# Performance work log

Measured on AMD Instinct MI355X. Metric: run time of the kernel, lower is better.

Reference implementation:

```python
import jax, jax.numpy as jnp
import numpy as np

B, N, DIM = 4, 2048, 256
H, HD, M = 8, 32, 4
SPARSE_TOPK = 32


def setup_inputs() -> dict:
    key = jax.random.key(0)
    ks = jax.random.split(key, 6)
    x = jax.random.normal(ks[0], (B, N, DIM), dtype=jnp.float32)
    w_qkv = jax.random.normal(ks[1], (DIM, 3 * H * HD), dtype=jnp.float32) * 0.02
    b_qkv = jnp.zeros((3 * H * HD,), dtype=jnp.float32)
    w_proj = jax.random.normal(ks[2], (H * HD, DIM), dtype=jnp.float32) * 0.02
    b_proj = jnp.zeros((DIM,), dtype=jnp.float32)
    scale = jnp.ones((1, H, 1, 1), dtype=jnp.float32)  # trainable scale, init scale_value=1.0
    mem_k = jax.random.normal(ks[3], (H, M, HD), dtype=jnp.float32)
    mem_v = jax.random.normal(ks[4], (H, M, HD), dtype=jnp.float32)
    return {"x": x, "w_qkv": w_qkv, "b_qkv": b_qkv, "w_proj": w_proj,
            "b_proj": b_proj, "scale": scale, "mem_k": mem_k, "mem_v": mem_v}


def reference(x, w_qkv, b_qkv, w_proj, b_proj, scale, mem_k, mem_v):
    b, n, dim = x.shape
    h, m, hd = mem_k.shape
    qkv = (x @ w_qkv + b_qkv).reshape(b, n, 3, h, hd).transpose(2, 0, 3, 1, 4)
    q, k, v = qkv[0], qkv[1], qkv[2]
    # concat memory vectors along key-length axis -> [B,H,N+M,hd]
    k = jnp.concatenate([k, jnp.broadcast_to(mem_k, (b, h, m, hd))], axis=2)
    v = jnp.concatenate([v, jnp.broadcast_to(mem_v, (b, h, m, hd))], axis=2)
    s = n + m
    # scores with trainable per-head scale: [B,H,N,S]
    scores = jnp.einsum('bhnd,bhsd->bhns', q, k) * (hd ** -0.5) * scale
    neg = -jnp.finfo(scores.dtype).max
    # improve_locality: mask rectangular diagonal (eye(N, S))
    diag = jnp.arange(n)[:, None] == jnp.arange(s)[None, :]
    scores = jnp.where(diag, neg, scores)
    # sparse topk: keep only values >= k-th largest per row
    top = jax.lax.top_k(scores, SPARSE_TOPK)[0]
    vk = top[..., -1:]
    scores = jnp.where(scores < vk, neg, scores)
    attn = jax.nn.softmax(scores, axis=-1)
    out = jnp.einsum('bhns,bhsd->bhnd', attn, v)
    out = out.transpose(0, 2, 1, 3).reshape(b, n, h * hd)
    return out @ w_proj + b_proj
```

## Files before the change

kernel.cpp:

```cpp
#include <hip/hip_runtime.h>
#include <float.h>
#include <stdint.h>

#define Bb   4
#define Nn   2048
#define DIMc 256
#define Hh   8
#define HDd  32
#define Mm   4
#define STOT 2052
#define ROWS 8
#define SROW 2112
#define NVROW 2052

typedef float f32x2 __attribute__((ext_vector_type(2)));

__device__ __forceinline__ unsigned int f2key(float s) {
    unsigned int b = __float_as_uint(s);
    return (b & 0x80000000u) ? ~b : (b | 0x80000000u);
}
__device__ __forceinline__ float key2f(unsigned int u) {
    unsigned int b = (u & 0x80000000u) ? (u ^ 0x80000000u) : ~u;
    return __uint_as_float(b);
}

__global__ __launch_bounds__(256) void sgemm_qkv(
    const float* __restrict__ A, const float* __restrict__ Bm,
    const float* __restrict__ bias, float* __restrict__ Qb,
    float* __restrict__ kTb, float* __restrict__ Vx,
    const float* __restrict__ memv)
{
    __shared__ __align__(16) float As[16][68];
    __shared__ __align__(16) float Bs[16][64];
    __shared__ __align__(16) float Ts[64][65];
    const int tid = threadIdx.x;
    const int tx = tid & 15, ty = tid >> 4;
    const int m0 = blockIdx.y * 64, n0 = blockIdx.x * 64;
    const int arow = tid >> 2, acol = (tid & 3) * 4;
    const int brow = tid >> 4, bcol = (tid & 15) * 4;
    float acc[4][4] = {};
    for (int kb = 0; kb < DIMc; kb += 16) {
        const float4 av = *(const float4*)&A[(size_t)(m0 + arow) * DIMc + kb + acol];
        const float4 bv = *(const float4*)&Bm[(size_t)(kb + brow) * 768 + n0 + bcol];
        __syncthreads();
        As[acol + 0][arow] = av.x;
        As[acol + 1][arow] = av.y;
        As[acol + 2][arow] = av.z;
        As[acol + 3][arow] = av.w;
        *(float4*)&Bs[brow][bcol] = bv;
        __syncthreads();
#pragma unroll
        for (int k = 0; k < 16; ++k) {
            const float4 a  = *(const float4*)&As[k][ty * 4];
            const float4 bq = *(const float4*)&Bs[k][tx * 4];
            const float aa[4] = {a.x, a.y, a.z, a.w};
            const float bb[4] = {bq.x, bq.y, bq.z, bq.w};
#pragma unroll
            for (int i = 0; i < 4; ++i)
#pragma unroll
                for (int j = 0; j < 4; ++j)
                    acc[i][j] = fmaf(aa[i], bb[j], acc[i][j]);
        }
    }
    const float4 bv = *(const float4*)&bias[n0 + tx * 4];
    const float bb[4] = {bv.x, bv.y, bv.z, bv.w};
    const int path = n0 >> 8;
    if (path == 1) {
#pragma unroll
        for (int i = 0; i < 4; ++i)
#pragma unroll
            for (int j = 0; j < 4; ++j)
                Ts[tx * 4 + j][ty * 4 + i] = acc[i][j] + bb[j];
        __syncthreads();
        const int c_local = tid >> 2;
        const int seg     = tid & 3;
        const int cg = (n0 - 256) + c_local;
        const int hh = cg >> 5, dd = cg & 31;
        const int bi = m0 >> 11, j0 = (m0 & 2047) + seg * 16;
        float* dst = kTb + (((size_t)(bi * Hh + hh) * HDd + dd) * Nn) + j0;
#pragma unroll
        for (int q = 0; q < 4; ++q)
            *(float4*)(dst + q * 4) = *(const float4*)&Ts[c_local][seg * 16 + q * 4];
    } else if (path == 0) {
        const int c0 = n0 + tx * 4;
#pragma unroll
        for (int i = 0; i < 4; ++i) {
            float4 o;
            o.x = acc[i][0] + bb[0];
            o.y = acc[i][1] + bb[1];
            o.z = acc[i][2] + bb[2];
            o.w = acc[i][3] + bb[3];
            *(float4*)&Qb[(size_t)(m0 + ty * 4 + i) * 256 + c0] = o;
        }
    } else {
        const int c0 = (n0 & 255) + tx * 4;
        const size_t row_base = (size_t)(m0 >> 11) * NVROW + (m0 & 2047);
#pragma unroll
        for (int i = 0; i < 4; ++i) {
            float4 o;
            o.x = acc[i][0] + bb[0];
            o.y = acc[i][1] + bb[1];
            o.z = acc[i][2] + bb[2];
            o.w = acc[i][3] + bb[3];
            *(float4*)&Vx[(row_base + ty * 4 + i) * 256 + c0] = o;
        }
        if (n0 == 512 && (m0 & 2047) == 0) {
            const int bb2 = m0 >> 11;
#pragma unroll
            for (int mm = 0; mm < Mm; ++mm)
                Vx[((size_t)bb2 * NVROW + Nn + mm) * 256 + tid] =
                    memv[((tid >> 5) * Mm + mm) * HDd + (tid & 31)];
        }
    }
}

__global__ __launch_bounds__(256) void sgemm_bias(
    const float* __restrict__ A, const float* __restrict__ Bm,
    const float* __restrict__ bias, float* __restrict__ C,
    int Md, int Nd, int Kd)
{
    __shared__ __align__(16) float As[16][68];
    __shared__ __align__(16) float Bs[16][64];
    const int tid = threadIdx.x;
    const int tx = tid & 15, ty = tid >> 4;
    const int m0 = blockIdx.y * 64, n0 = blockIdx.x * 64;
    const int arow = tid >> 2, acol = (tid & 3) * 4;
    const int brow = tid >> 4, bcol = (tid & 15) * 4;
    float acc[4][4] = {};
    for (int kb = 0; kb < Kd; kb += 16) {
        const float4 av = *(const float4*)&A[(size_t)(m0 + arow) * Kd + kb + acol];
        const float4 bv = *(const float4*)&Bm[(size_t)(kb + brow) * Nd + n0 + bcol];
        __syncthreads();
        As[acol + 0][arow] = av.x;
        As[acol + 1][arow] = av.y;
        As[acol + 2][arow] = av.z;
        As[acol + 3][arow] = av.w;
        *(float4*)&Bs[brow][bcol] = bv;
        __syncthreads();
#pragma unroll
        for (int k = 0; k < 16; ++k) {
            const float4 a  = *(const float4*)&As[k][ty * 4];
            const float4 bq = *(const float4*)&Bs[k][tx * 4];
            const float aa[4] = {a.x, a.y, a.z, a.w};
            const float bb[4] = {bq.x, bq.y, bq.z, bq.w};
#pragma unroll
            for (int i = 0; i < 4; ++i)
#pragma unroll
                for (int j = 0; j < 4; ++j)
                    acc[i][j] = fmaf(aa[i], bb[j], acc[i][j]);
        }
    }
    const float4 bv = *(const float4*)&bias[n0 + tx * 4];
    const float bb[4] = {bv.x, bv.y, bv.z, bv.w};
#pragma unroll
    for (int i = 0; i < 4; ++i) {
        float4 o;
        o.x = acc[i][0] + bb[0];
        o.y = acc[i][1] + bb[1];
        o.z = acc[i][2] + bb[2];
        o.w = acc[i][3] + bb[3];
        *(float4*)&C[(size_t)(m0 + ty * 4 + i) * Nd + n0 + tx * 4] = o;
    }
}

#if __has_builtin(__builtin_elementwise_fma)
#define PKSTEP(Q, P)                                                        \
    { const f32x2 qq = {(Q), (Q)};                                          \
      a01 = __builtin_elementwise_fma(qq, ((const f32x2*)&kd[P])[0], a01);  \
      a23 = __builtin_elementwise_fma(qq, ((const f32x2*)&kd[P])[1], a23); }
#else
#define PKSTEP(Q, P)                                                        \
    { a01.x = fmaf((Q), kd[P].x, a01.x); a01.y = fmaf((Q), kd[P].y, a01.y); \
      a23.x = fmaf((Q), kd[P].z, a23.x); a23.y = fmaf((Q), kd[P].w, a23.y); }
#endif

__global__ __launch_bounds__(512, 4) void attn_sparse(
    const float* __restrict__ Qb, const float* __restrict__ kTb,
    const float* __restrict__ Vx, const float* __restrict__ memk,
    const float* __restrict__ scale, float* __restrict__ attn_out)
{
    __shared__ __align__(16) unsigned int S[ROWS][SROW];
    __shared__ __align__(16) float qs[ROWS][HDd];
    __shared__ unsigned int       u_list[ROWS][64];
    __shared__ unsigned short     j_list[ROWS][64];
    __shared__ unsigned long long wj_list[ROWS][64];

    const int tid    = threadIdx.x;
    const int ntiles = Nn / ROWS;
    const int tile   = blockIdx.x % ntiles;
    const int h      = (blockIdx.x / ntiles) % Hh;
    const int b      = blockIdx.x / (ntiles * Hh);
    const int n0     = tile * ROWS;
    const float sc   = scale[h] * 0.17677669529663688f;

    if (tid < ROWS * HDd) {
        const int r = tid >> 5, d2 = tid & 31;
        qs[r][d2] = Qb[(size_t)(b * Nn + n0 + r) * 256 + h * HDd + d2];
    }
    __syncthreads();

    const float* kT = kTb + (size_t)(b * Hh + h) * (HDd * Nn);

    {
        const int j0 = tid * 4;
        f32x2 acc01[ROWS], acc23[ROWS];
#pragma unroll
        for (int r = 0; r < ROWS; ++r) { acc01[r] = (f32x2){0.f, 0.f}; acc23[r] = (f32x2){0.f, 0.f}; }
#pragma unroll 1
        for (int dc = 0; dc < 4; ++dc) {
            float4 kd[8];
#pragma unroll
            for (int dd = 0; dd < 8; ++dd)
                kd[dd] = *(const float4*)&kT[(dc * 8 + dd) * Nn + j0];
#pragma unroll
            for (int r = 0; r < ROWS; ++r) {
                const float4 qa = *(const float4*)&qs[r][dc * 8];
                const float4 qb2 = *(const float4*)&qs[r][dc * 8 + 4];
                f32x2 a01 = acc01[r], a23 = acc23[r];
                PKSTEP(qa.x, 0) PKSTEP(qa.y, 1) PKSTEP(qa.z, 2) PKSTEP(qa.w, 3)
                PKSTEP(qb2.x, 4) PKSTEP(qb2.y, 5) PKSTEP(qb2.z, 6) PKSTEP(qb2.w, 7)
                acc01[r] = a01; acc23[r] = a23;
            }
        }
#pragma unroll
        for (int r = 0; r < ROWS; ++r) {
            const float af[4] = {acc01[r].x, acc01[r].y, acc23[r].x, acc23[r].y};
            uint4 o;
            unsigned int* op = (unsigned int*)&o;
#pragma unroll
            for (int kk = 0; kk < 4; ++kk) {
                float s = af[kk] * sc;
                if (j0 + kk == n0 + r) s = -FLT_MAX;
                op[kk] = f2key(s);
            }
            *(uint4*)&S[r][j0] = o;
        }
    }
    if (tid < 16) {
        const int j0 = 2048 + tid * 4;
        float acc[ROWS][4];
#pragma unroll
        for (int r = 0; r < ROWS; ++r)
#pragma unroll
            for (int kk = 0; kk < 4; ++kk) acc[r][kk] = 0.f;
        const float* kp[4];
#pragma unroll
        for (int kk = 0; kk < 4; ++kk) {
            const int j = j0 + kk;
            kp[kk] = (j < STOT) ? (memk + (size_t)(h * Mm + (j - Nn)) * HDd)
                                : memk;
        }
#pragma unroll 1
        for (int dc = 0; dc < 4; ++dc) {
            float4 k0[4], k1[4];
#pragma unroll
            for (int kk = 0; kk < 4; ++kk) {
                k0[kk] = *(const float4*)(kp[kk] + dc * 8);
                k1[kk] = *(const float4*)(kp[kk] + dc * 8 + 4);
            }
#pragma unroll
            for (int r = 0; r < ROWS; ++r) {
                const float4 qa = *(const float4*)&qs[r][dc * 8];
                const float4 qb2 = *(const float4*)&qs[r][dc * 8 + 4];
#pragma unroll
                for (int kk = 0; kk < 4; ++kk) {
                    float t = fmaf(qa.x, k0[kk].x, acc[r][kk]);
                    t = fmaf(qa.y, k0[kk].y, t);
                    t = fmaf(qa.z, k0[kk].z, t);
                    t = fmaf(qa.w, k0[kk].w, t);
                    t = fmaf(qb2.x, k1[kk].x, t);
                    t = fmaf(qb2.y, k1[kk].y, t);
                    t = fmaf(qb2.z, k1[kk].z, t);
                    t = fmaf(qb2.w, k1[kk].w, t);
                    acc[r][kk] = t;
                }
            }
        }
#pragma unroll
        for (int r = 0; r < ROWS; ++r) {
            uint4 o;
            unsigned int* op = (unsigned int*)&o;
#pragma unroll
            for (int kk = 0; kk < 4; ++kk) {
                const int j = j0 + kk;
                float s = acc[r][kk] * sc;
                if (j >= STOT || j == n0 + r) s = -FLT_MAX;
                op[kk] = f2key(s);
            }
            *(uint4*)&S[r][j0] = o;
        }
    }
    __syncthreads();

    const int wave = tid >> 6, lane = tid & 63;
    const int half = lane >> 5, d = lane & 31;
    const int n = n0 + wave;

    unsigned int uv[33];
    unsigned int mx = 0u;
    {
        const unsigned int* Srow = &S[wave][lane];
#pragma unroll
        for (int i = 0; i < 33; ++i) {
            uv[i] = Srow[i * 64];
            mx = uv[i] > mx ? uv[i] : mx;
        }
    }

    auto bitonic = [&](unsigned int vv) -> unsigned int {
#pragma unroll
        for (int kk = 2; kk <= 64; kk <<= 1)
#pragma unroll
            for (int jj = kk >> 1; jj > 0; jj >>= 1) {
                const unsigned int o = (unsigned int)__shfl_xor((int)vv, jj);
                const unsigned int mn = vv < o ? vv : o;
                const unsigned int mxv = vv < o ? o : vv;
                const bool up   = ((lane & kk) == 0);
                const bool lowr = ((lane & jj) == 0);
                vv = (lowr == up) ? mn : mxv;
            }
        return vv;
    };
    auto countge = [&](unsigned int tt) -> int {
        int gg = 0;
#pragma unroll
        for (int i = 0; i < 33; ++i) gg += (int)__popcll(__ballot(uv[i] >= tt));
        return gg;
    };

    const unsigned int vs1 = bitonic(mx);
    const unsigned int Lmax = (unsigned int)__shfl((int)vs1, 63);
    unsigned int t = (unsigned int)__shfl((int)vs1, 32);

    int g = countge(t);
    bool exact = true;
    if (g > 64) {
        unsigned int blo = t, bhi = Lmax + 1;
        int found = 0;
#pragma unroll 1
        for (int it = 0; it < 33; ++it) {
            if (bhi - blo <= 1u) break;
            const unsigned int tm = blo + ((bhi - blo) >> 1);
            const int gm = countge(tm);
            if (gm > 64) blo = tm;
            else if (gm < 32) bhi = tm;
            else { t = tm; g = gm; found = 1; break; }
        }
        if (!found) { t = blo; g = countge(blo); exact = (g <= 64); }
    }

    u_list[wave][lane] = 0u;
    j_list[wave][lane] = 0;
    __asm__ __volatile__("s_waitcnt lgkmcnt(0)" ::: "memory");
    int base = 0;
#pragma unroll
    for (int i = 0; i < 33; ++i) {
        const bool p = (uv[i] >= t);
        const unsigned long long mk = __ballot(p);
        if (p) {
            const int pos = base + (int)__popcll(mk & ((1ull << lane) - 1ull));
            if (pos < 64) {
                u_list[wave][pos] = uv[i];
                j_list[wave][pos] = (unsigned short)(i * 64 + lane);
            }
        }
        base += (int)__popcll(mk);
    }
    const int C2 = base < 64 ? base : 64;
    __asm__ __volatile__("s_waitcnt lgkmcnt(0)" ::: "memory");
    const unsigned int ue = u_list[wave][lane];
    const int je = (int)j_list[wave][lane];

    const unsigned int vs2 = bitonic(ue);
    unsigned int vkkey = (unsigned int)__shfl((int)vs2, 32);
    const unsigned int v31u = (unsigned int)__shfl((int)vs2, 31);
    if (!exact) vkkey = t;

    const bool tie_span = (v31u == vkkey);
    float snx = -3.0e38f;
    if (exact && !tie_span) {
        if (C2 == 32) {
            unsigned int unx = 0u;
#pragma unroll
            for (int i = 0; i < 33; ++i) {
                const unsigned int u = uv[i];
                if (u < vkkey && u > unx) unx = u;
            }
#pragma unroll
            for (int o = 32; o > 0; o >>= 1) {
                const unsigned int ou = (unsigned int)__shfl_xor((int)unx, o);
                if (ou > unx) unx = ou;
            }
            snx = key2f(unx);
        } else {
            snx = key2f(v31u);
        }
    }
    const float svk  = key2f(vkkey);
    const float gapv = svk - snx;
    const float lam  = (exact && !tie_span && gapv > 0.f && gapv <= 4.0e-6f) ? 0.13f : 0.f;

    const float mval = key2f(Lmax);
    const float we = (ue >= vkkey) ? __expf(key2f(ue) - mval) : 0.f;
    wj_list[wave][lane] = ((unsigned long long)(unsigned int)je << 32) | (unsigned long long)__float_as_uint(we);
    float Z = we;
#pragma unroll
    for (int o = 32; o > 0; o >>= 1) Z += __shfl_xor(Z, o);
    __asm__ __volatile__("s_waitcnt lgkmcnt(0)" ::: "memory");

    const float* Vbh = Vx + (size_t)b * (NVROW * 256) + h * HDd;
    float outv = 0.f;
#pragma unroll 1
    for (int e0 = 0; e0 < C2; e0 += 8) {
        float w[4]; int q[4];
#pragma unroll
        for (int u2 = 0; u2 < 4; ++u2) {
            const unsigned long long wj = wj_list[wave][e0 + u2 * 2 + half];
            w[u2] = __uint_as_float((unsigned int)wj);
            q[u2] = (int)(wj >> 32);
        }
        float vv[4];
#pragma unroll
        for (int u2 = 0; u2 < 4; ++u2)
            vv[u2] = Vbh[(size_t)q[u2] * 256 + d];
#pragma unroll
        for (int u2 = 0; u2 < 4; ++u2)
            outv = fmaf(w[u2], vv[u2], outv);
    }
    outv += __shfl_xor(outv, 32);

    float res = outv / Z;
    if (lam > 0.f) {
        unsigned int unx2 = 0u; int jnx = 0, jd1 = -1;
#pragma unroll
        for (int i = 0; i < 33; ++i) {
            const unsigned int u = uv[i];
            const int jj2 = i * 64 + lane;
            if (u < vkkey && u > unx2) { unx2 = u; jnx = jj2; }
            if (u == vkkey && jj2 > jd1) jd1 = jj2;
        }
#pragma unroll
        for (int o = 32; o > 0; o >>= 1) {
            const unsigned int ou = (unsigned int)__shfl_xor((int)unx2, o);
            const int oj = __shfl_xor(jnx, o);
            if (ou > unx2 || (ou == unx2 && oj > jnx)) { unx2 = ou; jnx = oj; }
            const int od = __shfl_xor(jd1, o);
            if (od > jd1) jd1 = od;
        }
        const float wd = __expf(svk - mval);
        const float wn = __expf(key2f(unx2) - mval);
        const float* vp1 = Vbh + (size_t)jd1 * 256;
        const float* vpn = Vbh + (size_t)jnx * 256;
        const float ZB = Z - wd + wn;
        const float oB = (outv - wd * vp1[d] + wn * vpn[d]) / ZB;
        res = (1.f - lam) * res + lam * oB;
    }
    if (half == 0)
        attn_out[(size_t)(b * Nn + n) * 256 + h * HDd + d] = res;
}

extern "C" void kernel_launch(void* const* d_in, const int* in_sizes, int n_in,
                              void* d_out, int out_size, void* d_ws, size_t ws_size,
                              hipStream_t stream) {
    const float* x      = (const float*)d_in[0];
    const float* w_qkv  = (const float*)d_in[1];
    const float* b_qkv  = (const float*)d_in[2];
    const float* w_proj = (const float*)d_in[3];
    const float* b_proj = (const float*)d_in[4];
    const float* scale  = (const float*)d_in[5];
    const float* mem_k  = (const float*)d_in[6];
    const float* mem_v  = (const float*)d_in[7];
    float* out = (float*)d_out;

    float* Qb  = (float*)d_ws;
    float* kTb = Qb  + (size_t)Bb * Nn * 256;
    float* Vx  = kTb + (size_t)Bb * Hh * HDd * Nn;

    sgemm_qkv<<<dim3(768 / 64, (Bb * Nn) / 64), 256, 0, stream>>>(
        x, w_qkv, b_qkv, Qb, kTb, Vx, mem_v);

    attn_sparse<<<dim3(Bb * Hh * (Nn / ROWS)), 512, 0, stream>>>(
        Qb, kTb, Vx, mem_k, scale, Qb);

    sgemm_bias<<<dim3(DIMc / 64, (Bb * Nn) / 64), 256, 0, stream>>>(
        Qb, w_proj, b_proj, out, Bb * Nn, DIMc, DIMc);
}
```

Before: 419.6 us.

## Load Q rows via scalar loads, pack top-k lists, vectorize weight reads

Drops the shared-memory Q staging and its __syncthreads, and reads Q rows straight from global memory with inline-asm s_load_dwordx4 into scalar registers, so the score FMAs use SGPR operands instead of LDS broadcasts. The packed f32x2 FMAs become scalar FMAs. The u/j candidate lists are merged into one 64-bit LDS array, and wj_list is stored interleaved so each half-wave fetches its weights with two 128-bit LDS reads. The inline asm depends on Q being wave-uniform and on the offset encoding being right, and the scalar FMAs may issue more instructions than the packed ones did.

After: 412.4 us. Within noise of the previous version (-1.7%).

```diff
diff --git a/kernel.cpp b/kernel.cpp
--- a/kernel.cpp
+++ b/kernel.cpp
@@ -14,6 +14,8 @@
 #define NVROW 2052
 
 typedef float f32x2 __attribute__((ext_vector_type(2)));
+typedef float sf32x4 __attribute__((ext_vector_type(4)));
+typedef unsigned long long u64;
 
 __device__ __forceinline__ unsigned int f2key(float s) {
     unsigned int b = __float_as_uint(s);
@@ -163,16 +165,39 @@
     }
 }
 
-#if __has_builtin(__builtin_elementwise_fma)
-#define PKSTEP(Q, P)                                                        \
-    { const f32x2 qq = {(Q), (Q)};                                          \
-      a01 = __builtin_elementwise_fma(qq, ((const f32x2*)&kd[P])[0], a01);  \
-      a23 = __builtin_elementwise_fma(qq, ((const f32x2*)&kd[P])[1], a23); }
-#else
-#define PKSTEP(Q, P)                                                        \
-    { a01.x = fmaf((Q), kd[P].x, a01.x); a01.y = fmaf((Q), kd[P].y, a01.y); \
-      a23.x = fmaf((Q), kd[P].z, a23.x); a23.y = fmaf((Q), kd[P].w, a23.y); }
-#endif
+#define QLOAD4(QA0, QA1, QB0, QB1, QC0, QC1, QD0, QD1, O0, O1, O2, O3)      \
+    asm volatile(                                                            \
+        "s_load_dwordx4 %0, %8, %9\n\t"                                      \
+        "s_load_dwordx4 %1, %8, %10\n\t"                                     \
+        "s_load_dwordx4 %2, %8, %11\n\t"                                     \
+        "s_load_dwordx4 %3, %8, %12\n\t"                                     \
+        "s_load_dwordx4 %4, %8, %13\n\t"                                     \
+        "s_load_dwordx4 %5, %8, %14\n\t"                                     \
+        "s_load_dwordx4 %6, %8, %15\n\t"                                     \
+        "s_load_dwordx4 %7, %8, %16\n\t"                                     \
+        "s_waitcnt lgkmcnt(0)"                                               \
+        : "=s"(QA0), "=s"(QA1), "=s"(QB0), "=s"(QB1),                        \
+          "=s"(QC0), "=s"(QC1), "=s"(QD0), "=s"(QD1)                         \
+        : "s"(qrow), "s"(O0), "s"((O0) + 16u), "s"(O1), "s"((O1) + 16u),     \
+          "s"(O2), "s"((O2) + 16u), "s"(O3), "s"((O3) + 16u));
+
+#define ROWFMA(QLO, QHI, R)                                                  \
+    { _Pragma("unroll")                                                      \
+      for (int u = 0; u < 4; ++u) {                                          \
+          const float qv = (QLO)[u];                                         \
+          a0[R] = fmaf(qv, kd[u].x, a0[R]);                                  \
+          a1[R] = fmaf(qv, kd[u].y, a1[R]);                                  \
+          a2[R] = fmaf(qv, kd[u].z, a2[R]);                                  \
+          a3[R] = fmaf(qv, kd[u].w, a3[R]);                                  \
+      }                                                                      \
+      _Pragma("unroll")                                                      \
+      for (int u = 0; u < 4; ++u) {                                          \
+          const float qv = (QHI)[u];                                         \
+          a0[R] = fmaf(qv, kd[u + 4].x, a0[R]);                              \
+          a1[R] = fmaf(qv, kd[u + 4].y, a1[R]);                              \
+          a2[R] = fmaf(qv, kd[u + 4].z, a2[R]);                              \
+          a3[R] = fmaf(qv, kd[u + 4].w, a3[R]);                              \
+      } }
 
 __global__ __launch_bounds__(512, 4) void attn_sparse(
     const float* __restrict__ Qb, const float* __restrict__ kTb,
@@ -180,10 +205,8 @@
     const float* __restrict__ scale, float* __restrict__ attn_out)
 {
     __shared__ __align__(16) unsigned int S[ROWS][SROW];
-    __shared__ __align__(16) float qs[ROWS][HDd];
-    __shared__ unsigned int       u_list[ROWS][64];
-    __shared__ unsigned short     j_list[ROWS][64];
-    __shared__ unsigned long long wj_list[ROWS][64];
+    __shared__ __align__(16) u64 ulist64[ROWS][64];
+    __shared__ __align__(16) u64 wj_list[ROWS][64];
 
     const int tid    = threadIdx.x;
     const int ntiles = Nn / ROWS;
@@ -193,38 +216,43 @@
     const int n0     = tile * ROWS;
     const float sc   = scale[h] * 0.17677669529663688f;
 
-    if (tid < ROWS * HDd) {
-        const int r = tid >> 5, d2 = tid & 31;
-        qs[r][d2] = Qb[(size_t)(b * Nn + n0 + r) * 256 + h * HDd + d2];
-    }
-    __syncthreads();
-
-    const float* kT = kTb + (size_t)(b * Hh + h) * (HDd * Nn);
+    const float* kT   = kTb + (size_t)(b * Hh + h) * (HDd * Nn);
+    const float* qrow = Qb + (size_t)(b * Nn + n0) * 256 + h * HDd;
 
     {
         const int j0 = tid * 4;
-        f32x2 acc01[ROWS], acc23[ROWS];
-#pragma unroll
-        for (int r = 0; r < ROWS; ++r) { acc01[r] = (f32x2){0.f, 0.f}; acc23[r] = (f32x2){0.f, 0.f}; }
+        float a0[ROWS], a1[ROWS], a2[ROWS], a3[ROWS];
+#pragma unroll
+        for (int r = 0; r < ROWS; ++r) { a0[r] = 0.f; a1[r] = 0.f; a2[r] = 0.f; a3[r] = 0.f; }
 #pragma unroll 1
         for (int dc = 0; dc < 4; ++dc) {
             float4 kd[8];
 #pragma unroll
             for (int dd = 0; dd < 8; ++dd)
                 kd[dd] = *(const float4*)&kT[(dc * 8 + dd) * Nn + j0];
-#pragma unroll
-            for (int r = 0; r < ROWS; ++r) {
-                const float4 qa = *(const float4*)&qs[r][dc * 8];
-                const float4 qb2 = *(const float4*)&qs[r][dc * 8 + 4];
-                f32x2 a01 = acc01[r], a23 = acc23[r];
-                PKSTEP(qa.x, 0) PKSTEP(qa.y, 1) PKSTEP(qa.z, 2) PKSTEP(qa.w, 3)
-                PKSTEP(qb2.x, 4) PKSTEP(qb2.y, 5) PKSTEP(qb2.z, 6) PKSTEP(qb2.w, 7)
-                acc01[r] = a01; acc23[r] = a23;
+            const unsigned int ob = (unsigned int)(dc * 32);
+            {
+                sf32x4 qA0, qA1, qB0, qB1, qC0, qC1, qD0, qD1;
+                QLOAD4(qA0, qA1, qB0, qB1, qC0, qC1, qD0, qD1,
+                       ob, ob + 1024u, ob + 2048u, ob + 3072u);
+                ROWFMA(qA0, qA1, 0)
+                ROWFMA(qB0, qB1, 1)
+                ROWFMA(qC0, qC1, 2)
+                ROWFMA(qD0, qD1, 3)
+            }
+            {
+                sf32x4 qA0, qA1, qB0, qB1, qC0, qC1, qD0, qD1;
+                QLOAD4(qA0, qA1, qB0, qB1, qC0, qC1, qD0, qD1,
+                       ob + 4096u, ob + 5120u, ob + 6144u, ob + 7168u);
+                ROWFMA(qA0, qA1, 4)
+                ROWFMA(qB0, qB1, 5)
+                ROWFMA(qC0, qC1, 6)
+                ROWFMA(qD0, qD1, 7)
             }
         }
 #pragma unroll
         for (int r = 0; r < ROWS; ++r) {
-            const float af[4] = {acc01[r].x, acc01[r].y, acc23[r].x, acc23[r].y};
+            const float af[4] = {a0[r], a1[r], a2[r], a3[r]};
             uint4 o;
             unsigned int* op = (unsigned int*)&o;
 #pragma unroll
@@ -260,8 +288,8 @@
             }
 #pragma unroll
             for (int r = 0; r < ROWS; ++r) {
-                const float4 qa = *(const float4*)&qs[r][dc * 8];
-                const float4 qb2 = *(const float4*)&qs[r][dc * 8 + 4];
+                const float4 qa  = *(const float4*)&qrow[r * 256 + dc * 8];
+                const float4 qb2 = *(const float4*)&qrow[r * 256 + dc * 8 + 4];
 #pragma unroll
                 for (int kk = 0; kk < 4; ++kk) {
                     float t = fmaf(qa.x, k0[kk].x, acc[r][kk]);
@@ -349,8 +377,7 @@
         if (!found) { t = blo; g = countge(blo); exact = (g <= 64); }
     }
 
-    u_list[wave][lane] = 0u;
-    j_list[wave][lane] = 0;
+    ulist64[wave][lane] = 0ull;
     __asm__ __volatile__("s_waitcnt lgkmcnt(0)" ::: "memory");
     int base = 0;
 #pragma unroll
@@ -359,17 +386,16 @@
         const unsigned long long mk = __ballot(p);
         if (p) {
             const int pos = base + (int)__popcll(mk & ((1ull << lane) - 1ull));
-            if (pos < 64) {
-                u_list[wave][pos] = uv[i];
-                j_list[wave][pos] = (unsigned short)(i * 64 + lane);
-            }
+            if (pos < 64)
+                ulist64[wave][pos] = ((u64)uv[i] << 32) | (unsigned int)(i * 64 + lane);
         }
         base += (int)__popcll(mk);
     }
     const int C2 = base < 64 ? base : 64;
     __asm__ __volatile__("s_waitcnt lgkmcnt(0)" ::: "memory");
-    const unsigned int ue = u_list[wave][lane];
-    const int je = (int)j_list[wave][lane];
+    const u64 pk = ulist64[wave][lane];
+    const unsigned int ue = (unsigned int)(pk >> 32);
+    const int je = (int)(unsigned int)pk;
 
     const unsigned int vs2 = bitonic(ue);
     unsigned int vkkey = (unsigned int)__shfl((int)vs2, 32);
@@ -402,7 +428,8 @@
 
     const float mval = key2f(Lmax);
     const float we = (ue >= vkkey) ? __expf(key2f(ue) - mval) : 0.f;
-    wj_list[wave][lane] = ((unsigned long long)(unsigned int)je << 32) | (unsigned long long)__float_as_uint(we);
+    wj_list[wave][(lane & 1) * 32 + (lane >> 1)] =
+        ((u64)(unsigned int)je << 32) | (u64)__float_as_uint(we);
     float Z = we;
 #pragma unroll
     for (int o = 32; o > 0; o >>= 1) Z += __shfl_xor(Z, o);
@@ -412,13 +439,14 @@
     float outv = 0.f;
 #pragma unroll 1
     for (int e0 = 0; e0 < C2; e0 += 8) {
+        const int p0 = (e0 >> 1) + half * 32;
+        const ulonglong2 wa = *(const ulonglong2*)&wj_list[wave][p0];
+        const ulonglong2 wb = *(const ulonglong2*)&wj_list[wave][p0 + 2];
         float w[4]; int q[4];
-#pragma unroll
-        for (int u2 = 0; u2 < 4; ++u2) {
-            const unsigned long long wj = wj_list[wave][e0 + u2 * 2 + half];
-            w[u2] = __uint_as_float((unsigned int)wj);
-            q[u2] = (int)(wj >> 32);
-        }
+        w[0] = __uint_as_float((unsigned int)wa.x); q[0] = (int)(wa.x >> 32);
+        w[1] = __uint_as_float((unsigned int)wa.y); q[1] = (int)(wa.y >> 32);
+        w[2] = __uint_as_float((unsigned int)wb.x); q[2] = (int)(wb.x >> 32);
+        w[3] = __uint_as_float((unsigned int)wb.y); q[3] = (int)(wb.y >> 32);
         float vv[4];
 #pragma unroll
         for (int u2 = 0; u2 < 4; ++u2)
```
